# Kernel tuning notes

Hardware: AMD Instinct MI355X
Metric: run time of the kernel (lower is better)

## Reference

```python
import jax, jax.numpy as jnp
import numpy as np

D = 100        # persistence-image resolution (forced by CNN out: 32*25*25)
VAR = 0.5      # pers_im_var
B, P = 32, 128 # graphs, persistence pairs per graph
N, IN, HID = 16000, 128, 64
NUM_CLASSES = 10


def setup_inputs() -> dict:
    key = jax.random.key(0)
    ks = jax.random.split(key, 13)
    s = 0.05
    return {
        "x": jax.random.normal(ks[0], (N, IN), jnp.float32),
        "pair_idx0": jax.random.randint(ks[1], (B, P, 2), 0, N, jnp.int32),
        "pair_idx1": jax.random.randint(ks[2], (B, P, 2), 0, N, jnp.int32),
        "w1": jax.random.normal(ks[3], (IN, HID), jnp.float32) * s,
        "b1": jnp.zeros((HID,), jnp.float32),
        "w2": jax.random.normal(ks[4], (HID, 1), jnp.float32) * s,
        "b2": jnp.zeros((1,), jnp.float32),
        "conv1_w": jax.random.normal(ks[5], (16, 2, 5, 5), jnp.float32) * s,
        "conv1_b": jnp.zeros((16,), jnp.float32),
        "conv2_w": jax.random.normal(ks[6], (32, 16, 5, 5), jnp.float32) * s,
        "conv2_b": jnp.zeros((32,), jnp.float32),
        "out_w": jax.random.normal(ks[7], (NUM_CLASSES, 32 * 25 * 25), jnp.float32) * s,
        "out_b": jnp.zeros((NUM_CLASSES,), jnp.float32),
    }


def _pers_image(bd):
    # bd: [B, P, 2] birth/death filtration values
    # bdpt_to_bdps = [[1,-1],[0,1]] : (b, d) -> (b, d - b)
    birth = bd[..., 0]
    pers = bd[..., 1] - bd[..., 0]
    coords = jnp.arange(D, dtype=bd.dtype) / D  # arange(0, 0.999, 1/D) -> D pts
    # Gaussian over 2D grid; axis i <-> birth coord, axis j <-> persistence coord
    g = (birth[:, :, None, None] - coords[None, None, :, None]) ** 2 \
        + (pers[:, :, None, None] - coords[None, None, None, :]) ** 2
    im = jnp.exp(-g / (2.0 * VAR)) / (2.0 * jnp.pi * VAR)  # [B, P, D, D]
    im = im.sum(axis=1)  # sum over points -> [B, D, D]
    im = im / im.max(axis=(1, 2), keepdims=True)  # per-sample normalization
    return im


def _conv(x, w, b):
    y = jax.lax.conv_general_dilated(
        x, w, window_strides=(1, 1), padding=((2, 2), (2, 2)),
        dimension_numbers=("NCHW", "OIHW", "NCHW"))
    return y + b[None, :, None, None]


def _maxpool2(x):
    return jax.lax.reduce_window(x, -jnp.inf, jax.lax.max,
                                 (1, 1, 2, 2), (1, 1, 2, 2), "VALID")


def reference(x, pair_idx0, pair_idx1, w1, b1, w2, b2,
              conv1_w, conv1_b, conv2_w, conv2_b, out_w, out_b):
    # Linear_fil: Linear -> ReLU -> Linear -> Sigmoid -> squeeze
    h = jax.nn.relu(x @ w1 + b1)
    node_filt = jax.nn.sigmoid(h @ w2 + b2)[:, 0]  # [N]

    # persistence pairs as gathers of vertex filtration values (diff. path of ph)
    h0 = node_filt[pair_idx0]  # [B, P, 2]
    h1 = node_filt[pair_idx1]  # [B, P, 2]

    im0 = _pers_image(h0)
    im1 = _pers_image(h1)
    imgs = jnp.stack([im0, im1], axis=1)  # [B, 2, D, D]

    # CNN head
    y = _maxpool2(jax.nn.relu(_conv(imgs, conv1_w, conv1_b)))  # [B,16,50,50]
    y = _maxpool2(jax.nn.relu(_conv(y, conv2_w, conv2_b)))     # [B,32,25,25]
    y = y.reshape(y.shape[0], -1)
    y_hat = y @ out_w.T + out_b  # [B, num_classes]
    return (y_hat, node_filt)
```

## Files before the change

### kernel.cpp

```cpp
#include <hip/hip_runtime.h>
#include <hip/hip_bf16.h>

#define N_NODES 16000
#define IN_F 128
#define HID 64
#define BATCH 32
#define NPAIR 128
#define DRES 100
#define NCLS 10

#define NF_OFF     0
#define WT1_OFF    16000
#define WT2B_OFF   16800
#define INV_OFF    23200
#define MAXB_OFF   23264
#define IMGSP_OFF  23328
#define POOL1P_OFF 715552
#define POOL2_OFF  2263840
#define ZERO_N4    560144

#define NFILT_BLK  125
#define NZBLK      548

#define PV(P, r, c) (((c) & 1) ? P[(r)*3 + ((c)>>1)].y : P[(r)*3 + ((c)>>1)].x)

typedef short short8 __attribute__((ext_vector_type(8)));
typedef float f32x16 __attribute__((ext_vector_type(16)));

static __device__ __forceinline__ unsigned short f2b(float f) {
    __hip_bfloat16 h = __float2bfloat16(f);
    return *reinterpret_cast<unsigned short*>(&h);
}
static __device__ __forceinline__ unsigned int pk2(float a, float b) {
    return (unsigned int)f2b(a) | ((unsigned int)f2b(b) << 16);
}

#define COFF(k) (((k)/25)*336 + (((k)%25)/5)*56 + ((k)%25)%5)

__global__ __launch_bounds__(256) void k_initfilt(
    const float* __restrict__ x, const float* __restrict__ w1,
    const float* __restrict__ b1, const float* __restrict__ w2,
    const float* __restrict__ b2, float* __restrict__ nf, float* __restrict__ out_nf,
    const float* __restrict__ c1w, const float* __restrict__ c2w,
    float* __restrict__ wT1, unsigned int* __restrict__ wT2b,
    float* __restrict__ zbase)
{
    int bx = blockIdx.x, t = threadIdx.x;
    if (bx < NFILT_BLK) {
        int wave = t >> 6, lane = t & 63;
        int n0 = (bx * 4 + wave) * 32;
        int hh = lane >> 5, sm = lane & 31;
        const float* xr = x + (size_t)(n0 + sm) * IN_F + hh * 8;
        const float* wbase = w1 + hh * 512 + sm;

        f32x16 acc0 = {0.f,0.f,0.f,0.f,0.f,0.f,0.f,0.f,0.f,0.f,0.f,0.f,0.f,0.f,0.f,0.f};
        f32x16 acc1 = {0.f,0.f,0.f,0.f,0.f,0.f,0.f,0.f,0.f,0.f,0.f,0.f,0.f,0.f,0.f,0.f};

        #pragma unroll
        for (int s = 0; s < 8; ++s) {
            float4 v0 = *(const float4*)(xr + s * 16);
            float4 v1 = *(const float4*)(xr + s * 16 + 4);
            union { short8 v; unsigned int u[4]; } a;
            a.u[0] = pk2(v0.x, v0.y);
            a.u[1] = pk2(v0.z, v0.w);
            a.u[2] = pk2(v1.x, v1.y);
            a.u[3] = pk2(v1.z, v1.w);
            union { short8 v; unsigned int u[4]; } b0f, b1f;
            #pragma unroll
            for (int r = 0; r < 4; ++r) {
                float wa0 = wbase[s * 1024 + r * 128];
                float wb0 = wbase[s * 1024 + r * 128 + 64];
                float wa1 = wbase[s * 1024 + r * 128 + 32];
                float wb1v = wbase[s * 1024 + r * 128 + 96];
                b0f.u[r] = pk2(wa0, wb0);
                b1f.u[r] = pk2(wa1, wb1v);
            }
            acc0 = __builtin_amdgcn_mfma_f32_32x32x16_bf16(a.v, b0f.v, acc0, 0, 0, 0);
            acc1 = __builtin_amdgcn_mfma_f32_32x32x16_bf16(a.v, b1f.v, acc1, 0, 0, 0);
        }

        int h0 = sm, h1 = 32 + sm;
        float b10 = b1[h0], b11 = b1[h1], w20 = w2[h0], w21 = w2[h1];
        float q[16];
        #pragma unroll
        for (int r = 0; r < 16; ++r)
            q[r] = fmaxf(acc0[r] + b10, 0.f) * w20 + fmaxf(acc1[r] + b11, 0.f) * w21;
        #pragma unroll
        for (int off = 1; off < 32; off <<= 1) {
            #pragma unroll
            for (int r = 0; r < 16; ++r)
                q[r] += __shfl_xor(q[r], off, 64);
        }
        if (sm == 0) {
            float b2v = b2[0];
            #pragma unroll
            for (int r = 0; r < 16; ++r) {
                int m = (r & 3) + 8 * (r >> 2) + 4 * hh;
                float f = 1.f / (1.f + expf(-(q[r] + b2v)));
                nf[n0 + m] = f;
                out_nf[n0 + m] = f;
            }
        }
        return;
    }
    if (bx == NFILT_BLK) {
        for (int i = t; i < 800; i += 256) {
            int ic = i / 400, tap = (i / 16) % 25, oc = i % 16;
            wT1[i] = c1w[(oc * 2 + ic) * 25 + tap];
        }
        return;
    }
    if (bx == NFILT_BLK + 1) {
        for (int i = t; i < 6400; i += 256) {
            int kp = i >> 5, oc = i & 31;
            int k0 = 2 * kp, k1 = k0 + 1;
            float f0 = c2w[(oc * 16 + k0 / 25) * 25 + k0 % 25];
            float f1 = c2w[(oc * 16 + k1 / 25) * 25 + k1 % 25];
            wT2b[i] = pk2(f0, f1);
        }
        return;
    }
    int zi = (bx - (NFILT_BLK + 2)) * 1024 + t;
    float4 z = make_float4(0.f, 0.f, 0.f, 0.f);
    #pragma unroll
    for (int r = 0; r < 4; ++r) {
        int i = zi + r * 256;
        if (i < ZERO_N4) ((float4*)zbase)[i] = z;
    }
}

__global__ __launch_bounds__(256) void k_pimg(const float* __restrict__ nf,
    const int* __restrict__ pi0, const int* __restrict__ pi1,
    float* __restrict__ imgs_p, unsigned int* __restrict__ maxb)
{
    int g = blockIdx.x;
    int img = (g & 7) * 8 + ((g >> 3) & 7);
    int q = g >> 6;
    int b = img >> 1, c = img & 1;
    const int* pi = c ? pi1 : pi0;
    __shared__ float sb[NPAIR], sp[NPAIR];
    __shared__ float wm[4];
    int t = threadIdx.x;
    if (t < NPAIR) {
        int i0 = pi[(b * NPAIR + t) * 2 + 0];
        int i1 = pi[(b * NPAIR + t) * 2 + 1];
        float f0 = nf[i0], f1 = nf[i1];
        sb[t] = f0;
        sp[t] = f1 - f0;
    }
    __syncthreads();
    bool act = t < 169;
    int ti = t / 13, tj = t % 13;
    float acc[8][2] = {};
    if (act) {
        float ci[8];
        #pragma unroll
        for (int r = 0; r < 8; ++r) ci[r] = (float)(ti + 13 * r) * 0.01f;
        float cj0 = (float)(q * 25 + tj) * 0.01f;
        float cj1 = (float)(q * 25 + tj + 13) * 0.01f;
        for (int p = 0; p < NPAIR; ++p) {
            float bb = sb[p], pp = sp[p];
            float d0 = pp - cj0, d1 = pp - cj1;
            float e0 = __expf(-d0 * d0), e1 = __expf(-d1 * d1);
            #pragma unroll
            for (int r = 0; r < 8; ++r) {
                float d = bb - ci[r];
                float eb = __expf(-d * d);
                acc[r][0] = fmaf(eb, e0, acc[r][0]);
                acc[r][1] = fmaf(eb, e1, acc[r][1]);
            }
        }
    }
    float lmax = 0.f;
    if (act) {
        float* dst = imgs_p + (size_t)img * 10816 + 2 * 104 + 2 + q * 25;
        #pragma unroll
        for (int r = 0; r < 8; ++r) {
            int i = ti + 13 * r;
            if (i < DRES) {
                dst[i * 104 + tj] = acc[r][0];
                lmax = fmaxf(lmax, acc[r][0]);
                if (tj < 12) {
                    dst[i * 104 + tj + 13] = acc[r][1];
                    lmax = fmaxf(lmax, acc[r][1]);
                }
            }
        }
    }
    #pragma unroll
    for (int off = 32; off > 0; off >>= 1)
        lmax = fmaxf(lmax, __shfl_xor(lmax, off, 64));
    if ((t & 63) == 0) wm[t >> 6] = lmax;
    __syncthreads();
    if (t == 0) {
        float bm = fmaxf(fmaxf(wm[0], wm[1]), fmaxf(wm[2], wm[3]));
        atomicMax(&maxb[img], __float_as_uint(bm));
    }
}

__global__ __launch_bounds__(256) void k_conv1(const float* __restrict__ imgs_p,
    const float* __restrict__ wT1, const float* __restrict__ cb,
    const unsigned int* __restrict__ maxb, float* __restrict__ pool1p)
{
    int g = blockIdx.x;
    int b = (g & 7) * 4 + ((g >> 3) & 3);
    int ocg = (g >> 5) & 3;
    int rg = g >> 7;
    int t = threadIdx.x;
    if (t >= 250) return;
    int ow = t % 50, oh = rg * 5 + t / 50;

    float2 PA[18], PB[18];
    {
        const float* bs = imgs_p + (size_t)(b * 2 + 0) * 10816 + (2 * oh) * 104 + 2 * ow;
        #pragma unroll
        for (int r = 0; r < 6; ++r) {
            const float* rp = bs + r * 104;
            PA[r * 3 + 0] = *(const float2*)rp;
            PA[r * 3 + 1] = *(const float2*)(rp + 2);
            PA[r * 3 + 2] = *(const float2*)(rp + 4);
        }
        const float* bs1 = bs + 10816;
        #pragma unroll
        for (int r = 0; r < 6; ++r) {
            const float* rp = bs1 + r * 104;
            PB[r * 3 + 0] = *(const float2*)rp;
            PB[r * 3 + 1] = *(const float2*)(rp + 2);
            PB[r * 3 + 2] = *(const float2*)(rp + 4);
        }
    }
    float acc0[4][2][2] = {}, acc1[4][2][2] = {};
    const float* w0 = wT1 + ocg * 4;
    const float* w1r = wT1 + 400 + ocg * 4;
    #pragma unroll
    for (int kh = 0; kh < 5; ++kh)
        #pragma unroll
        for (int kw = 0; kw < 5; ++kw) {
            float4 wa = *(const float4*)(w0 + (kh * 5 + kw) * 16);
            float4 wb = *(const float4*)(w1r + (kh * 5 + kw) * 16);
            #pragma unroll
            for (int j = 0; j < 2; ++j)
                #pragma unroll
                for (int i = 0; i < 2; ++i) {
                    float va = PV(PA, kh + j, kw + i);
                    float vb = PV(PB, kh + j, kw + i);
                    acc0[0][j][i] = fmaf(va, wa.x, acc0[0][j][i]);
                    acc0[1][j][i] = fmaf(va, wa.y, acc0[1][j][i]);
                    acc0[2][j][i] = fmaf(va, wa.z, acc0[2][j][i]);
                    acc0[3][j][i] = fmaf(va, wa.w, acc0[3][j][i]);
                    acc1[0][j][i] = fmaf(vb, wb.x, acc1[0][j][i]);
                    acc1[1][j][i] = fmaf(vb, wb.y, acc1[1][j][i]);
                    acc1[2][j][i] = fmaf(vb, wb.z, acc1[2][j][i]);
                    acc1[3][j][i] = fmaf(vb, wb.w, acc1[3][j][i]);
                }
        }
    float sc0 = 1.f / __uint_as_float(maxb[b * 2 + 0]);
    float sc1 = 1.f / __uint_as_float(maxb[b * 2 + 1]);
    float4 bias4 = *(const float4*)(cb + ocg * 4);
    float bv[4] = {bias4.x, bias4.y, bias4.z, bias4.w};
    #pragma unroll
    for (int o = 0; o < 4; ++o) {
        float v00 = fmaf(sc1, acc1[o][0][0], sc0 * acc0[o][0][0]);
        float v01 = fmaf(sc1, acc1[o][0][1], sc0 * acc0[o][0][1]);
        float v10 = fmaf(sc1, acc1[o][1][0], sc0 * acc0[o][1][0]);
        float v11 = fmaf(sc1, acc1[o][1][1], sc0 * acc0[o][1][1]);
        float m = fmaxf(fmaxf(v00, v01), fmaxf(v10, v11));
        pool1p[((size_t)(b * 16 + ocg * 4 + o) * 54 + oh + 2) * 56 + ow + 2] =
            fmaxf(m + bv[o], 0.f);
    }
}

__global__ __launch_bounds__(128) void k_conv2(const float* __restrict__ pool1p,
    const unsigned int* __restrict__ wg, const float* __restrict__ cb2,
    float* __restrict__ pool2)
{
    int g = blockIdx.x;
    int b = (g & 7) * 4 + ((g >> 3) & 3);
    int py = g >> 5;
    int t = threadIdx.x;

    __shared__ unsigned short inb[5376];
    {
        const float* src = pool1p + (size_t)b * 48384 + (2 * py) * 56;
        unsigned int* inb32 = (unsigned int*)inb;
        for (int i = t; i < 1344; i += 128) {
            int ic = i / 84, rem = i % 84;
            int r = rem / 14, c4 = rem % 14;
            float4 v = *(const float4*)(src + ic * 3024 + r * 56 + c4 * 4);
            inb32[i * 2 + 0] = pk2(v.x, v.y);
            inb32[i * 2 + 1] = pk2(v.z, v.w);
        }
    }
    __syncthreads();

    int lane = t & 63;
    int h = t >> 6;
    int hh = lane >> 5;
    int sm = lane & 31;
    int cb = h * 32 + sm; if (cb > 49) cb = 49;
    int cbA = cb, cbB = cb + 56;
    int oc = sm;
    int wbase = hh * 128 + oc;

    f32x16 accA = {0.f,0.f,0.f,0.f,0.f,0.f,0.f,0.f,0.f,0.f,0.f,0.f,0.f,0.f,0.f,0.f};
    f32x16 accB = {0.f,0.f,0.f,0.f,0.f,0.f,0.f,0.f,0.f,0.f,0.f,0.f,0.f,0.f,0.f,0.f};

    #pragma unroll
    for (int s = 0; s < 25; ++s) {
        union { short8 v; unsigned int u[4]; } bw;
        bw.u[0] = wg[wbase + s * 256 + 0];
        bw.u[1] = wg[wbase + s * 256 + 32];
        bw.u[2] = wg[wbase + s * 256 + 64];
        bw.u[3] = wg[wbase + s * 256 + 96];
        unsigned short ua[8], ub[8];
        #pragma unroll
        for (int e = 0; e < 8; ++e) {
            int o = hh ? COFF(16 * s + 8 + e) : COFF(16 * s + e);
            ua[e] = inb[cbA + o];
            ub[e] = inb[cbB + o];
        }
        union { short8 v; unsigned int u[4]; } aA, aB;
        #pragma unroll
        for (int r = 0; r < 4; ++r) {
            aA.u[r] = (unsigned int)ua[2 * r] | ((unsigned int)ua[2 * r + 1] << 16);
            aB.u[r] = (unsigned int)ub[2 * r] | ((unsigned int)ub[2 * r + 1] << 16);
        }
        accA = __builtin_amdgcn_mfma_f32_32x32x16_bf16(aA.v, bw.v, accA, 0, 0, 0);
        accB = __builtin_amdgcn_mfma_f32_32x32x16_bf16(aB.v, bw.v, accB, 0, 0, 0);
    }

    float bias = cb2[oc];
    float* dst = pool2 + ((size_t)(b * 32 + oc) * 25 + py) * 25;
    #pragma unroll
    for (int q = 0; q < 4; ++q) {
        float m0 = fmaxf(fmaxf(accA[4 * q + 0], accB[4 * q + 0]),
                         fmaxf(accA[4 * q + 1], accB[4 * q + 1]));
        float m1 = fmaxf(fmaxf(accA[4 * q + 2], accB[4 * q + 2]),
                         fmaxf(accA[4 * q + 3], accB[4 * q + 3]));
        int px0 = h * 16 + 4 * q + 2 * hh;
        if (px0 < 25) dst[px0] = fmaxf(m0 + bias, 0.f);
        if (px0 + 1 < 25) dst[px0 + 1] = fmaxf(m1 + bias, 0.f);
    }
}

__global__ __launch_bounds__(256) void k_fc(const float* __restrict__ pool2,
    const float* __restrict__ oww, const float* __restrict__ ob,
    float* __restrict__ yhat)
{
    int cls = blockIdx.x / BATCH, b = blockIdx.x % BATCH;
    int t = threadIdx.x;
    const float4* y = (const float4*)(pool2 + (size_t)b * 20000);
    const float4* w = (const float4*)(oww + (size_t)cls * 20000);
    float acc = 0.f;
    for (int k = t; k < 5000; k += 256) {
        float4 a = y[k], ww = w[k];
        acc += a.x * ww.x + a.y * ww.y + a.z * ww.z + a.w * ww.w;
    }
    #pragma unroll
    for (int off = 32; off > 0; off >>= 1)
        acc += __shfl_xor(acc, off, 64);
    __shared__ float part[4];
    if ((t & 63) == 0) part[t >> 6] = acc;
    __syncthreads();
    if (t == 0)
        yhat[b * NCLS + cls] = part[0] + part[1] + part[2] + part[3] + ob[cls];
}

extern "C" void kernel_launch(void* const* d_in, const int* in_sizes, int n_in,
                              void* d_out, int out_size, void* d_ws, size_t ws_size,
                              hipStream_t stream)
{
    const float* x   = (const float*)d_in[0];
    const int*   pi0 = (const int*)d_in[1];
    const int*   pi1 = (const int*)d_in[2];
    const float* w1  = (const float*)d_in[3];
    const float* b1  = (const float*)d_in[4];
    const float* w2  = (const float*)d_in[5];
    const float* b2  = (const float*)d_in[6];
    const float* c1w = (const float*)d_in[7];
    const float* c1b = (const float*)d_in[8];
    const float* c2w = (const float*)d_in[9];
    const float* c2b = (const float*)d_in[10];
    const float* oww = (const float*)d_in[11];
    const float* owb = (const float*)d_in[12];
    float* out = (float*)d_out;
    float* ws = (float*)d_ws;

    float*        nf     = ws + NF_OFF;
    float*        wT1    = ws + WT1_OFF;
    unsigned int* wT2b   = (unsigned int*)(ws + WT2B_OFF);
    unsigned int* maxb   = (unsigned int*)(ws + MAXB_OFF);
    float*        imgs_p = ws + IMGSP_OFF;
    float*        pool1p = ws + POOL1P_OFF;
    float*        pool2  = ws + POOL2_OFF;

    k_initfilt<<<NFILT_BLK + 2 + NZBLK, 256, 0, stream>>>(
        x, w1, b1, w2, b2, nf, out + BATCH * NCLS,
        c1w, c2w, wT1, wT2b, ws + MAXB_OFF);
    k_pimg <<<256, 256, 0, stream>>>(nf, pi0, pi1, imgs_p, maxb);
    k_conv1<<<1280, 256, 0, stream>>>(imgs_p, wT1, c1b, maxb, pool1p);
    k_conv2<<<800, 128, 0, stream>>>(pool1p, wT2b, c2b, pool2);
    k_fc   <<<BATCH * NCLS, 256, 0, stream>>>(pool2, oww, owb, out);
}
```

Before: 65.82 us.

## Rewrite conv1 as bf16 MFMA implicit GEMM with LDS-staged input rows

Conv1 moves from per-thread fp32 FMA register tiling to an implicit GEMM on 32x32x16 bf16 MFMA instructions. Each block stages six padded input rows for both channels into shared memory as bf16, with the per-image max normalization folded in before packing. Weights are prepacked into A fragments (K padded from 50 to 64), and 2x2 max-pooling is done with lane shuffles on the accumulators. The aim is to cut the FMA-bound conv1 cost, at the price of bf16 rounding on inputs and weights, scalar LDS gathers with possible bank conflicts, and idle padded lanes and columns.

```diff
diff --git a/kernel.cpp b/kernel.cpp
--- a/kernel.cpp
+++ b/kernel.cpp
@@ -10,7 +10,7 @@
 #define NCLS 10
 
 #define NF_OFF     0
-#define WT1_OFF    16000
+#define WA1_OFF    16000
 #define WT2B_OFF   16800
 #define INV_OFF    23200
 #define MAXB_OFF   23264
@@ -22,8 +22,6 @@
 #define NFILT_BLK  125
 #define NZBLK      548
 
-#define PV(P, r, c) (((c) & 1) ? P[(r)*3 + ((c)>>1)].y : P[(r)*3 + ((c)>>1)].x)
-
 typedef short short8 __attribute__((ext_vector_type(8)));
 typedef float f32x16 __attribute__((ext_vector_type(16)));
 
@@ -36,13 +34,14 @@
 }
 
 #define COFF(k) (((k)/25)*336 + (((k)%25)/5)*56 + ((k)%25)%5)
+#define C1OFF(k) ((k) < 50 ? ((k)/25)*624 + ((((k)%25)/5))*104 + (((k)%25)%5) : 1248)
 
 __global__ __launch_bounds__(256) void k_initfilt(
     const float* __restrict__ x, const float* __restrict__ w1,
     const float* __restrict__ b1, const float* __restrict__ w2,
     const float* __restrict__ b2, float* __restrict__ nf, float* __restrict__ out_nf,
     const float* __restrict__ c1w, const float* __restrict__ c2w,
-    float* __restrict__ wT1, unsigned int* __restrict__ wT2b,
+    unsigned int* __restrict__ wA1, unsigned int* __restrict__ wT2b,
     float* __restrict__ zbase)
 {
     int bx = blockIdx.x, t = threadIdx.x;
@@ -104,9 +103,12 @@
         return;
     }
     if (bx == NFILT_BLK) {
-        for (int i = t; i < 800; i += 256) {
-            int ic = i / 400, tap = (i / 16) % 25, oc = i % 16;
-            wT1[i] = c1w[(oc * 2 + ic) * 25 + tap];
+        for (int i = t; i < 512; i += 256) {
+            int r = i & 3, m = (i >> 2) & 15, kg = (i >> 6) & 1, s = i >> 7;
+            int k0 = s * 16 + kg * 8 + 2 * r;
+            float f0 = (k0 < 50) ? c1w[m * 50 + k0] : 0.f;
+            float f1 = (k0 + 1 < 50) ? c1w[m * 50 + k0 + 1] : 0.f;
+            wA1[i] = pk2(f0, f1);
         }
         return;
     }
@@ -198,75 +200,90 @@
     }
 }
 
-__global__ __launch_bounds__(256) void k_conv1(const float* __restrict__ imgs_p,
-    const float* __restrict__ wT1, const float* __restrict__ cb,
+__global__ __launch_bounds__(128) void k_conv1(const float* __restrict__ imgs_p,
+    const unsigned int* __restrict__ wA1, const float* __restrict__ cb1,
     const unsigned int* __restrict__ maxb, float* __restrict__ pool1p)
 {
     int g = blockIdx.x;
     int b = (g & 7) * 4 + ((g >> 3) & 3);
-    int ocg = (g >> 5) & 3;
-    int rg = g >> 7;
+    int py = g >> 5;
     int t = threadIdx.x;
-    if (t >= 250) return;
-    int ow = t % 50, oh = rg * 5 + t / 50;
-
-    float2 PA[18], PB[18];
+
+    __shared__ unsigned short inbz[1472];
     {
-        const float* bs = imgs_p + (size_t)(b * 2 + 0) * 10816 + (2 * oh) * 104 + 2 * ow;
-        #pragma unroll
-        for (int r = 0; r < 6; ++r) {
-            const float* rp = bs + r * 104;
-            PA[r * 3 + 0] = *(const float2*)rp;
-            PA[r * 3 + 1] = *(const float2*)(rp + 2);
-            PA[r * 3 + 2] = *(const float2*)(rp + 4);
-        }
-        const float* bs1 = bs + 10816;
-        #pragma unroll
-        for (int r = 0; r < 6; ++r) {
-            const float* rp = bs1 + r * 104;
-            PB[r * 3 + 0] = *(const float2*)rp;
-            PB[r * 3 + 1] = *(const float2*)(rp + 2);
-            PB[r * 3 + 2] = *(const float2*)(rp + 4);
-        }
-    }
-    float acc0[4][2][2] = {}, acc1[4][2][2] = {};
-    const float* w0 = wT1 + ocg * 4;
-    const float* w1r = wT1 + 400 + ocg * 4;
-    #pragma unroll
-    for (int kh = 0; kh < 5; ++kh)
-        #pragma unroll
-        for (int kw = 0; kw < 5; ++kw) {
-            float4 wa = *(const float4*)(w0 + (kh * 5 + kw) * 16);
-            float4 wb = *(const float4*)(w1r + (kh * 5 + kw) * 16);
-            #pragma unroll
-            for (int j = 0; j < 2; ++j)
+        float sc0 = 1.f / __uint_as_float(maxb[b * 2 + 0]);
+        float sc1 = 1.f / __uint_as_float(maxb[b * 2 + 1]);
+        const float* s0 = imgs_p + (size_t)(b * 2 + 0) * 10816 + (2 * py) * 104;
+        const float* s1 = s0 + 10816;
+        unsigned int* z32 = (unsigned int*)inbz;
+        for (int i = t; i < 736; i += 128) {
+            unsigned int val = 0u;
+            if (i < 312) {
+                int s2 = 2 * i; int r = s2 / 104, cc = s2 % 104;
+                float2 v = *(const float2*)(s0 + r * 104 + cc);
+                val = pk2(v.x * sc0, v.y * sc0);
+            } else if (i < 624) {
+                int s2 = 2 * i - 624; int r = s2 / 104, cc = s2 % 104;
+                float2 v = *(const float2*)(s1 + r * 104 + cc);
+                val = pk2(v.x * sc1, v.y * sc1);
+            }
+            z32[i] = val;
+        }
+    }
+    __syncthreads();
+
+    int lane = t & 63;
+    int h = t >> 6;
+    int hh = lane >> 5;
+    int sm = lane & 31;
+    int q = lane & 3;
+    int cl = sm >> 2;
+    int laneoff = (q >> 1) * 104 + 2 * cl + (q & 1);
+
+    uint4 z4 = {0u, 0u, 0u, 0u};
+    union { short8 v; uint4 qd; } afr[4];
+    #pragma unroll
+    for (int s = 0; s < 4; ++s)
+        afr[s].qd = (sm < 16) ? *(const uint4*)(wA1 + ((s * 2 + hh) * 16 + sm) * 4) : z4;
+
+    float bb[8];
+    #pragma unroll
+    for (int r = 0; r < 8; ++r)
+        bb[r] = cb1[(r & 3) + 8 * (r >> 2) + 4 * hh];
+
+    #pragma unroll
+    for (int tt = 0; tt < 4; ++tt) {
+        int t_ = h + 2 * tt;
+        if (t_ < 7) {
+            const unsigned short* bp = inbz + laneoff + 16 * t_;
+            f32x16 acc = {0.f,0.f,0.f,0.f,0.f,0.f,0.f,0.f,0.f,0.f,0.f,0.f,0.f,0.f,0.f,0.f};
+            #pragma unroll
+            for (int s = 0; s < 4; ++s) {
+                unsigned short ub[8];
                 #pragma unroll
-                for (int i = 0; i < 2; ++i) {
-                    float va = PV(PA, kh + j, kw + i);
-                    float vb = PV(PB, kh + j, kw + i);
-                    acc0[0][j][i] = fmaf(va, wa.x, acc0[0][j][i]);
-                    acc0[1][j][i] = fmaf(va, wa.y, acc0[1][j][i]);
-                    acc0[2][j][i] = fmaf(va, wa.z, acc0[2][j][i]);
-                    acc0[3][j][i] = fmaf(va, wa.w, acc0[3][j][i]);
-                    acc1[0][j][i] = fmaf(vb, wb.x, acc1[0][j][i]);
-                    acc1[1][j][i] = fmaf(vb, wb.y, acc1[1][j][i]);
-                    acc1[2][j][i] = fmaf(vb, wb.z, acc1[2][j][i]);
-                    acc1[3][j][i] = fmaf(vb, wb.w, acc1[3][j][i]);
+                for (int e = 0; e < 8; ++e) {
+                    int off = hh ? C1OFF(16 * s + 8 + e) : C1OFF(16 * s + e);
+                    ub[e] = bp[off];
                 }
-        }
-    float sc0 = 1.f / __uint_as_float(maxb[b * 2 + 0]);
-    float sc1 = 1.f / __uint_as_float(maxb[b * 2 + 1]);
-    float4 bias4 = *(const float4*)(cb + ocg * 4);
-    float bv[4] = {bias4.x, bias4.y, bias4.z, bias4.w};
-    #pragma unroll
-    for (int o = 0; o < 4; ++o) {
-        float v00 = fmaf(sc1, acc1[o][0][0], sc0 * acc0[o][0][0]);
-        float v01 = fmaf(sc1, acc1[o][0][1], sc0 * acc0[o][0][1]);
-        float v10 = fmaf(sc1, acc1[o][1][0], sc0 * acc0[o][1][0]);
-        float v11 = fmaf(sc1, acc1[o][1][1], sc0 * acc0[o][1][1]);
-        float m = fmaxf(fmaxf(v00, v01), fmaxf(v10, v11));
-        pool1p[((size_t)(b * 16 + ocg * 4 + o) * 54 + oh + 2) * 56 + ow + 2] =
-            fmaxf(m + bv[o], 0.f);
+                union { short8 v; unsigned int u[4]; } bf;
+                #pragma unroll
+                for (int r = 0; r < 4; ++r)
+                    bf.u[r] = (unsigned int)ub[2 * r] | ((unsigned int)ub[2 * r + 1] << 16);
+                acc = __builtin_amdgcn_mfma_f32_32x32x16_bf16(afr[s].v, bf.v, acc, 0, 0, 0);
+            }
+            int pc = 8 * t_ + cl;
+            #pragma unroll
+            for (int r = 0; r < 8; ++r) {
+                float vr = acc[r];
+                vr = fmaxf(vr, __shfl_xor(vr, 1, 64));
+                vr = fmaxf(vr, __shfl_xor(vr, 2, 64));
+                if (q == 0 && pc < 50) {
+                    int oc = (r & 3) + 8 * (r >> 2) + 4 * hh;
+                    pool1p[((size_t)(b * 16 + oc) * 54 + py + 2) * 56 + pc + 2] =
+                        fmaxf(vr + bb[r], 0.f);
+                }
+            }
+        }
     }
 }
 
@@ -387,7 +404,7 @@
     float* ws = (float*)d_ws;
 
     float*        nf     = ws + NF_OFF;
-    float*        wT1    = ws + WT1_OFF;
+    unsigned int* wA1    = (unsigned int*)(ws + WA1_OFF);
     unsigned int* wT2b   = (unsigned int*)(ws + WT2B_OFF);
     unsigned int* maxb   = (unsigned int*)(ws + MAXB_OFF);
     float*        imgs_p = ws + IMGSP_OFF;
@@ -396,9 +413,9 @@
 
     k_initfilt<<<NFILT_BLK + 2 + NZBLK, 256, 0, stream>>>(
         x, w1, b1, w2, b2, nf, out + BATCH * NCLS,
-        c1w, c2w, wT1, wT2b, ws + MAXB_OFF);
+        c1w, c2w, wA1, wT2b, ws + MAXB_OFF);
     k_pimg <<<256, 256, 0, stream>>>(nf, pi0, pi1, imgs_p, maxb);
-    k_conv1<<<1280, 256, 0, stream>>>(imgs_p, wT1, c1b, maxb, pool1p);
+    k_conv1<<<1600, 128, 0, stream>>>(imgs_p, wA1, c1b, maxb, pool1p);
     k_conv2<<<800, 128, 0, stream>>>(pool1p, wT2b, c2b, pool2);
     k_fc   <<<BATCH * NCLS, 256, 0, stream>>>(pool2, oww, owb, out);
 }
```

New measurement: 66.83 us. No clear change (+1.5%).
